# Kernel optimization log

Hardware: AMD Instinct MI355X
Metric: run time of the kernel (lower is better)

The kernel has to match this reference:

```python
import jax, jax.numpy as jnp
import numpy as np

B, T, D_MODEL = 2, 2048, 2048
N_HEAD, N_KV = 16, 4
HEAD_DIM = D_MODEL // N_HEAD  # 128
N_REP = N_HEAD // N_KV        # 4
ROPE_BASE = 10000.0


def setup_inputs() -> dict:
    key = jax.random.key(0)
    ks = jax.random.split(key, 5)
    s = 0.02
    return {
        "x": jax.random.normal(ks[0], (B, T, D_MODEL), dtype=jnp.float32),
        "Wq": jax.random.normal(ks[1], (D_MODEL, N_HEAD * HEAD_DIM), dtype=jnp.float32) * s,
        "Wk": jax.random.normal(ks[2], (D_MODEL, N_KV * HEAD_DIM), dtype=jnp.float32) * s,
        "Wv": jax.random.normal(ks[3], (D_MODEL, N_KV * HEAD_DIM), dtype=jnp.float32) * s,
        "Wo": jax.random.normal(ks[4], (D_MODEL, D_MODEL), dtype=jnp.float32) * s,
    }


def _rope_cos_sin(seq_len, dim, dtype):
    inv_freq = 1.0 / (ROPE_BASE ** (jnp.arange(0, dim, 2, dtype=jnp.float32) / dim))
    t = jnp.arange(seq_len, dtype=jnp.float32)
    freqs = t[:, None] * inv_freq[None, :]          # (T, dim/2)
    emb = jnp.concatenate([freqs, freqs], axis=-1)  # (T, dim)
    return jnp.cos(emb).astype(dtype), jnp.sin(emb).astype(dtype)


def _rotate_half(x):
    half = x.shape[-1] // 2
    return jnp.concatenate([-x[..., half:], x[..., :half]], axis=-1)


def reference(x, Wq, Wk, Wv, Wo):
    Bx, Tx, _ = x.shape
    # projections (weights stored (in, out); equals torch Linear with W^T)
    q = (x @ Wq).reshape(Bx, Tx, N_HEAD, HEAD_DIM).transpose(0, 2, 1, 3)  # (B,H,T,d)
    k = (x @ Wk).reshape(Bx, Tx, N_KV, HEAD_DIM).transpose(0, 2, 1, 3)    # (B,Hkv,T,d)
    v = (x @ Wv).reshape(Bx, Tx, N_KV, HEAD_DIM).transpose(0, 2, 1, 3)

    cos, sin = _rope_cos_sin(Tx, HEAD_DIM, x.dtype)  # (T, d)
    q = q * cos + _rotate_half(q) * sin
    k = k * cos + _rotate_half(k) * sin

    # grouped attention: q grouped by kv head, avoids materializing repeated K/V
    qg = q.reshape(Bx, N_KV, N_REP, Tx, HEAD_DIM)
    scale = 1.0 / np.sqrt(HEAD_DIM)
    att = jnp.einsum('bgrtd,bgsd->bgrts', qg, k) * scale  # (B,Hkv,rep,T,S)
    causal = jnp.tril(jnp.ones((Tx, Tx), dtype=bool))
    att = jnp.where(causal, att, -jnp.inf)
    att = jax.nn.softmax(att, axis=-1)
    y = jnp.einsum('bgrts,bgsd->bgrtd', att, v)           # (B,Hkv,rep,T,d)
    y = y.reshape(Bx, N_HEAD, Tx, HEAD_DIM).transpose(0, 2, 1, 3).reshape(Bx, Tx, D_MODEL)
    return y @ Wo
```

## Files before the change

kernel.cpp:

```cpp
#include <hip/hip_runtime.h>
#include <hip/hip_bf16.h>

typedef unsigned short u16;
typedef unsigned int u32;
typedef __attribute__((ext_vector_type(4))) float f32x4;
typedef __attribute__((ext_vector_type(8))) __bf16 bf16x8;

#define B_   2
#define T_   2048
#define DM   2048
#define NH   16
#define NKV  4
#define HD   128

__device__ __forceinline__ u16 f2bf(float f){
    u32 u = __builtin_bit_cast(u32, f);
    u += 0x7FFFu + ((u >> 16) & 1u);
    return (u16)(u >> 16);
}

__device__ __forceinline__ void gld_lds16(const void* g, void* l){
    __builtin_amdgcn_global_load_lds(
        (const __attribute__((address_space(1))) void*)g,
        (__attribute__((address_space(3))) void*)l, 16, 0, 0);
}

__global__ void cast_v4(const float* __restrict__ in, u16* __restrict__ out){
    int i = blockIdx.x * 256 + threadIdx.x;
    float4 v = ((const float4*)in)[i];
    ushort4 o;
    o.x = f2bf(v.x); o.y = f2bf(v.y); o.z = f2bf(v.z); o.w = f2bf(v.w);
    ((ushort4*)out)[i] = o;
}

__global__ void transAll(const float* __restrict__ Wq, const float* __restrict__ Wk,
                         const float* __restrict__ Wv, const float* __restrict__ Wo,
                         u16* __restrict__ Wqkv, u16* __restrict__ Wot){
    __shared__ float tile[32][33];
    int bx = blockIdx.x;
    const float* W; u16* Out; int N; int nb; int perm;
    if (bx < 64)      { W = Wq; Out = Wqkv;                  N = 2048; nb = bx;      perm = 1; }
    else if (bx < 80) { W = Wk; Out = Wqkv + 2048ull * 2048; N = 512;  nb = bx - 64; perm = 1; }
    else if (bx < 96) { W = Wv; Out = Wqkv + 2560ull * 2048; N = 512;  nb = bx - 80; perm = 0; }
    else              { W = Wo; Out = Wot;                   N = 2048; nb = bx - 96; perm = 0; }
    int n0 = nb * 32, k0 = blockIdx.y * 32;
    int tx = threadIdx.x, ty = threadIdx.y;
#pragma unroll
    for (int i = 0; i < 4; i++)
        tile[ty + i * 8][tx] = W[(size_t)(k0 + ty + i * 8) * N + n0 + tx];
    __syncthreads();
#pragma unroll
    for (int i = 0; i < 4; i++){
        int n = n0 + ty + i * 8;
        int np = perm ? ((n & ~127) | ((n & 63) << 1) | ((n >> 6) & 1)) : n;
        Out[(size_t)np * 2048 + k0 + tx] = f2bf(tile[tx][ty + i * 8]);
    }
}

__global__ void rope_tab(float2* __restrict__ tab){
    int idx = blockIdx.x * 256 + threadIdx.x;
    int i = idx & 63, t = idx >> 6;
    float ang = (float)t * exp2f((float)i * (-13.287712379549449f / 64.0f));
    float sv, cv;
    __sincosf(ang, &sv, &cv);
    tab[idx] = make_float2(cv, sv);
}

#define BARR() { __builtin_amdgcn_s_barrier(); __builtin_amdgcn_sched_barrier(0); }
#define LGKM0() { asm volatile("s_waitcnt lgkmcnt(0)" ::: "memory"); __builtin_amdgcn_sched_barrier(0); }
#define VM4() { asm volatile("s_waitcnt vmcnt(4)" ::: "memory"); __builtin_amdgcn_sched_barrier(0); }

#define READ_A(QA, BUF) { \
    const char* ab = (const char*)&As[BUF][wm][0]; \
    _Pragma("unroll") for (int i = 0; i < 4; i++){ \
        int rh = ((QA)*4 + i)*16 + lx; \
        _Pragma("unroll") for (int ks = 0; ks < 2; ks++) \
            a_[i][ks] = *(const bf16x8*)(ab + rh*128 + (((ks*4+tg)*16) ^ ((lx&7)<<4))); \
    } }
#define READ_B(QB, BUF) { \
    const char* bb = (const char*)&Bs[BUF][wn>>1][0]; \
    _Pragma("unroll") for (int n = 0; n < 2; n++){ \
        int rbh = (wn&1)*64 + ((QB)*2+n)*16 + lx; \
        _Pragma("unroll") for (int ks = 0; ks < 2; ks++) \
            b_[(QB)*2+n][ks] = *(const bf16x8*)(bb + rbh*128 + (((ks*4+tg)*16) ^ ((lx&7)<<4))); \
    } }
#define MFMA_Q(QA, QB) { \
    __builtin_amdgcn_s_setprio(1); \
    _Pragma("unroll") for (int i = 0; i < 4; i++) \
    _Pragma("unroll") for (int n = 0; n < 2; n++) \
    _Pragma("unroll") for (int ks = 0; ks < 2; ks++) \
        acc[(QA)*4+i][(QB)*2+n] = __builtin_amdgcn_mfma_f32_16x16x32_bf16( \
            a_[i][ks], b_[(QB)*2+n][ks], acc[(QA)*4+i][(QB)*2+n], 0, 0, 0); \
    __builtin_amdgcn_s_setprio(0); }

template<int MODE>
__global__ __launch_bounds__(512, 2) void gemm256(const u16* __restrict__ A, const u16* __restrict__ Bt,
                                                  void* __restrict__ O0, u16* __restrict__ Ktl,
                                                  u16* __restrict__ Vtl, const float2* __restrict__ tab,
                                                  int NBX){
    __shared__ __attribute__((aligned(16))) u16 As[2][2][8192];
    __shared__ __attribute__((aligned(16))) u16 Bs[2][2][8192];
    const int tid = threadIdx.x;
    const int lane = tid & 63, w = tid >> 6;
    const int wm = w >> 2, wn = w & 3;
    const int tg = lane >> 4, lx = lane & 15;
    int q8 = (int)gridDim.x >> 3;
    int swz = ((int)blockIdx.x & 7) * q8 + ((int)blockIdx.x >> 3);
    const int bx = swz % NBX, by = swz / NBX;
    const int m0 = by * 256, n0 = bx * 256;
    const int K = 2048;
    const int kcx = (lane & 7) ^ ((lane >> 3) & 7);

    f32x4 acc[8][4];
    const f32x4 Z = {0.f, 0.f, 0.f, 0.f};
#pragma unroll
    for (int i = 0; i < 8; i++)
#pragma unroll
        for (int j = 0; j < 4; j++) acc[i][j] = Z;
    bf16x8 a_[4][2], b_[4][2];

    auto stA = [&](int buf, int q, int kt){
        int mh = w >> 2;
        int s0 = (w & 3) * 2;
#pragma unroll
        for (int l = 0; l < 2; l++){
            int s = s0 + l;
            gld_lds16(A + (size_t)(m0 + mh*128 + q*64 + s*8 + (lane>>3)) * K + kt*64 + kcx*8,
                      &As[buf][mh][q*4096 + s*512 + lane*8]);
        }
    };
    auto stB = [&](int buf, int q, int kt){
        int bh = w >> 2;
        int hi = (w >> 1) & 1;
        int s0 = (w & 1) * 2;
#pragma unroll
        for (int l = 0; l < 2; l++){
            int s = s0 + l;
            gld_lds16(Bt + (size_t)(n0 + bh*128 + hi*64 + q*32 + s*8 + (lane>>3)) * K + kt*64 + kcx*8,
                      &Bs[buf][bh][hi*4096 + q*2048 + s*512 + lane*8]);
        }
    };

    stA(0, 0, 0); stB(0, 0, 0); stA(0, 1, 0); stB(0, 1, 0);
    stA(1, 0, 1); stB(1, 0, 1);
    VM4(); BARR();

#pragma unroll 1
    for (int it = 0; it < 16; it++){
        const int T1 = 2*it + 1;
        const int T2 = (2*it + 2 < 32) ? 2*it + 2 : 31;
        const int T3 = (2*it + 3 < 32) ? 2*it + 3 : 31;
        READ_A(0, 0); READ_B(0, 0); stA(1, 1, T1);
        BARR(); LGKM0(); MFMA_Q(0, 0); BARR();
        READ_B(1, 0); stB(1, 1, T1);
        BARR(); LGKM0(); MFMA_Q(0, 1); BARR();
        READ_A(1, 0); stA(0, 0, T2);
        BARR(); LGKM0(); MFMA_Q(1, 0); BARR();
        stB(0, 0, T2);
        BARR(); MFMA_Q(1, 1); VM4(); BARR();
        READ_A(0, 1); READ_B(0, 1); stA(0, 1, T2);
        BARR(); LGKM0(); MFMA_Q(0, 0); BARR();
        READ_B(1, 1); stB(0, 1, T2);
        BARR(); LGKM0(); MFMA_Q(0, 1); BARR();
        READ_A(1, 1); stA(1, 0, T3);
        BARR(); LGKM0(); MFMA_Q(1, 0); BARR();
        stB(1, 0, T3);
        BARR(); MFMA_Q(1, 1); VM4(); BARR();
    }

    if constexpr (MODE == 0){
        float* C = (float*)O0;
#pragma unroll
        for (int mi = 0; mi < 8; mi++)
#pragma unroll
            for (int ni = 0; ni < 4; ni++){
                int r0 = m0 + wm*128 + mi*16 + tg*4;
                int c  = n0 + wn*64 + ni*16 + lx;
#pragma unroll
                for (int j = 0; j < 4; j++)
                    C[(size_t)(r0 + j) * 2048 + c] = acc[mi][ni][j];
            }
    } else {
        u16* Qp = (u16*)O0;
        if (bx < 8){
#pragma unroll
            for (int mi = 0; mi < 8; mi++)
#pragma unroll
                for (int ni = 0; ni < 4; ni++){
                    int r0 = m0 + wm*128 + mi*16 + tg*4;
                    int c  = n0 + wn*64 + ni*16 + lx;
                    int ii = (c & 127) >> 1;
#pragma unroll
                    for (int j = 0; j < 4; j++){
                        float v = acc[mi][ni][j];
                        float p = __shfl_xor(v, 1);
                        int t = (r0 + j) & 2047;
                        float2 cs = tab[t * 64 + ii];
                        float o = (lx & 1) ? (v * cs.x + p * cs.y) : (v * cs.x - p * cs.y);
                        Qp[(size_t)(r0 + j) * 2048 + c] = f2bf(o);
                    }
                }
        } else if (bx < 10){
#pragma unroll
            for (int mi = 0; mi < 8; mi++)
#pragma unroll
                for (int ni = 0; ni < 4; ni++){
                    int r0 = m0 + wm*128 + mi*16 + tg*4;
                    int c  = n0 + wn*64 + ni*16 + lx;
                    int hk = (c >> 7) & 3;
                    int dd = c & 127;
                    int ii = dd >> 1;
#pragma unroll
                    for (int j = 0; j < 4; j++){
                        int r = r0 + j;
                        int bb2 = r >> 11, tt = r & 2047;
                        float v = acc[mi][ni][j];
                        float p = __shfl_xor(v, 1);
                        float2 cs = tab[tt * 64 + ii];
                        float o = (lx & 1) ? (v * cs.x + p * cs.y) : (v * cs.x - p * cs.y);
                        size_t tb = ((size_t)(bb2 * 4 + hk) * 32 + (tt >> 6)) * 8192;
                        u32 byte = (u32)((tt & 63) * 256) + (((u32)(2 * dd)) ^ ((u32)((tt & 7) << 4)));
                        Ktl[tb + byte / 2] = f2bf(o);
                    }
                }
        } else {
#pragma unroll
            for (int mi = 0; mi < 8; mi++){
                int r0 = m0 + wm*128 + mi*16 + tg*4;
                int bb2 = r0 >> 11, ss = r0 & 2047;
#pragma unroll
                for (int ni = 0; ni < 4; ni++){
                    int c  = n0 + wn*64 + ni*16 + lx;
                    int hk = (c >> 7) & 3;
                    int d  = c & 127;
                    size_t tb = ((size_t)(bb2 * 4 + hk) * 32 + (ss >> 6)) * 8192;
                    u32 byte = (u32)(d * 128) + (((u32)((ss & 63) * 2)) ^ ((u32)((d & 7) << 4)));
                    ushort4 o;
                    o.x = f2bf(acc[mi][ni][0]); o.y = f2bf(acc[mi][ni][1]);
                    o.z = f2bf(acc[mi][ni][2]); o.w = f2bf(acc[mi][ni][3]);
                    *(ushort4*)(Vtl + tb + byte / 2) = o;
                }
            }
        }
    }
}

__global__ __launch_bounds__(256) void attn4(const u16* __restrict__ Q, const u16* __restrict__ Kt,
                                             const u16* __restrict__ Vt, u16* __restrict__ Y){
    __shared__ __attribute__((aligned(16))) u16 Ks[2][64 * 128];
    __shared__ __attribute__((aligned(16))) u16 Vs[2][64 * 128];
    __shared__ __attribute__((aligned(16))) u16 Pl[4][16 * 64];
    const int lane = threadIdx.x & 63, w = threadIdx.x >> 6;
    const int jb = blockIdx.x, h = blockIdx.y, b = blockIdx.z;
    const int hkv = h >> 2;
    const size_t kvBase = ((size_t)(b * NKV + hkv) * 32) * 8192;
    const float scale = 0.08838834764831845f;
    const f32x4 Z = {0.f, 0.f, 0.f, 0.f};
    const int tg = lane >> 4, lx = lane & 15;

    auto STAGE = [&](int buf, int it){
        const u16* kg = Kt + kvBase + (size_t)it * 8192;
        const u16* vg = Vt + kvBase + (size_t)it * 8192;
#pragma unroll
        for (int i = 0; i < 4; i++){
            int is = w * 4 + i;
            gld_lds16(kg + is * 512 + lane * 8, &Ks[buf][is * 512]);
            gld_lds16(vg + is * 512 + lane * 8, &Vs[buf][is * 512]);
        }
    };

#pragma unroll 1
    for (int pass = 0; pass < 2; pass++){
        const int qt = pass == 0 ? jb : 31 - jb;
        const int q0 = qt * 64;
        const int qrow = q0 + w * 16 + lx;
        bf16x8 qfr[4];
#pragma unroll
        for (int kk = 0; kk < 4; kk++)
            qfr[kk] = *(const bf16x8*)(Q + (size_t)(b * T_ + qrow) * DM + h * HD + kk * 32 + tg * 8);
        f32x4 accO[8];
#pragma unroll
        for (int i = 0; i < 8; i++) accO[i] = Z;
        float mr[4] = {-INFINITY, -INFINITY, -INFINITY, -INFINITY};
        float lp[4] = {0.f, 0.f, 0.f, 0.f};
        const int nIter = qt + 1;

        STAGE(0, 0);
        __syncthreads();
        int cur = 0;

#pragma unroll 1
        for (int it = 0; it < nIter; it++){
            if (it + 1 < nIter) STAGE(cur ^ 1, it + 1);
            f32x4 sa[4];
#pragma unroll
            for (int c = 0; c < 4; c++) sa[c] = Z;
            __builtin_amdgcn_s_setprio(1);
#pragma unroll
            for (int c = 0; c < 4; c++){
                int s = c * 16 + lx;
                u32 swz = (u32)((s & 7) << 4);
                const char* kb = (const char*)&Ks[cur][0] + s * 256;
#pragma unroll
                for (int kk = 0; kk < 4; kk++){
                    bf16x8 kf = *(const bf16x8*)(kb + (((u32)(kk * 64 + tg * 16)) ^ swz));
                    sa[c] = __builtin_amdgcn_mfma_f32_16x16x32_bf16(qfr[kk], kf, sa[c], 0, 0, 0);
                }
            }
            __builtin_amdgcn_s_setprio(0);
            const bool diag = (it == nIter - 1);
            float rmax[4];
#pragma unroll
            for (int j = 0; j < 4; j++){
                float a0 = sa[0][j] * scale, a1 = sa[1][j] * scale;
                float a2 = sa[2][j] * scale, a3 = sa[3][j] * scale;
                if (diag){
                    int qloc = w * 16 + tg * 4 + j;
                    if (lx      > qloc) a0 = -INFINITY;
                    if (lx + 16 > qloc) a1 = -INFINITY;
                    if (lx + 32 > qloc) a2 = -INFINITY;
                    if (lx + 48 > qloc) a3 = -INFINITY;
                }
                sa[0][j] = a0; sa[1][j] = a1; sa[2][j] = a2; sa[3][j] = a3;
                float t = fmaxf(fmaxf(a0, a1), fmaxf(a2, a3));
                t = fmaxf(t, __shfl_xor(t, 1));
                t = fmaxf(t, __shfl_xor(t, 2));
                t = fmaxf(t, __shfl_xor(t, 4));
                t = fmaxf(t, __shfl_xor(t, 8));
                rmax[j] = t;
            }
            int lok = (rmax[0] <= mr[0] + 8.f) && (rmax[1] <= mr[1] + 8.f) &&
                      (rmax[2] <= mr[2] + 8.f) && (rmax[3] <= mr[3] + 8.f);
            const bool ok = __all(lok);
            float corr[4];
#pragma unroll
            for (int j = 0; j < 4; j++){
                float mn;
                if (!ok){
                    mn = fmaxf(mr[j], rmax[j]);
                    corr[j] = __expf(mr[j] - mn);
                    mr[j] = mn;
                } else {
                    mn = mr[j];
                }
                float p0 = __expf(sa[0][j] - mn), p1 = __expf(sa[1][j] - mn);
                float p2 = __expf(sa[2][j] - mn), p3 = __expf(sa[3][j] - mn);
                int rr = tg * 4 + j;
                u32 swz = (u32)((rr & 7) << 4);
                char* pb = (char*)&Pl[w][0] + rr * 128;
                u32 cb = (u32)(lx * 2);
                *(u16*)(pb + ((cb      ) ^ swz)) = f2bf(p0);
                *(u16*)(pb + ((cb + 32 ) ^ swz)) = f2bf(p1);
                *(u16*)(pb + ((cb + 64 ) ^ swz)) = f2bf(p2);
                *(u16*)(pb + ((cb + 96 ) ^ swz)) = f2bf(p3);
                lp[j] = (ok ? lp[j] : lp[j] * corr[j]) + (p0 + p1 + p2 + p3);
            }
            if (!ok){
#pragma unroll
                for (int dt = 0; dt < 8; dt++){
                    f32x4 t = accO[dt];
                    t[0] *= corr[0]; t[1] *= corr[1]; t[2] *= corr[2]; t[3] *= corr[3];
                    accO[dt] = t;
                }
            }
            bf16x8 pf[2];
            {
                char* pb = (char*)&Pl[w][0] + lx * 128;
                u32 swz = (u32)((lx & 7) << 4);
                pf[0] = *(const bf16x8*)(pb + (((u32)(tg * 16))      ^ swz));
                pf[1] = *(const bf16x8*)(pb + (((u32)(tg * 16 + 64)) ^ swz));
            }
            __builtin_amdgcn_s_setprio(1);
#pragma unroll
            for (int dt = 0; dt < 8; dt++){
                int d = dt * 16 + lx;
                u32 swz = (u32)((d & 7) << 4);
                const char* vb = (const char*)&Vs[cur][0] + d * 128;
                bf16x8 vf0 = *(const bf16x8*)(vb + (((u32)(tg * 16))      ^ swz));
                bf16x8 vf1 = *(const bf16x8*)(vb + (((u32)(tg * 16 + 64)) ^ swz));
                accO[dt] = __builtin_amdgcn_mfma_f32_16x16x32_bf16(pf[0], vf0, accO[dt], 0, 0, 0);
                accO[dt] = __builtin_amdgcn_mfma_f32_16x16x32_bf16(pf[1], vf1, accO[dt], 0, 0, 0);
            }
            __builtin_amdgcn_s_setprio(0);
            __syncthreads();
            cur ^= 1;
        }
        float inv[4];
#pragma unroll
        for (int j = 0; j < 4; j++){
            float s = lp[j];
            s += __shfl_xor(s, 1);
            s += __shfl_xor(s, 2);
            s += __shfl_xor(s, 4);
            s += __shfl_xor(s, 8);
            inv[j] = 1.0f / s;
        }
#pragma unroll
        for (int dt = 0; dt < 8; dt++)
#pragma unroll
            for (int j = 0; j < 4; j++){
                int qr = q0 + w * 16 + tg * 4 + j;
                int d = dt * 16 + lx;
                Y[(size_t)(b * T_ + qr) * DM + h * HD + d] = f2bf(accO[dt][j] * inv[j]);
            }
    }
}

extern "C" void kernel_launch(void* const* d_in, const int* in_sizes, int n_in,
                              void* d_out, int out_size, void* d_ws, size_t ws_size,
                              hipStream_t stream){
    const float* x  = (const float*)d_in[0];
    const float* Wq = (const float*)d_in[1];
    const float* Wk = (const float*)d_in[2];
    const float* Wv = (const float*)d_in[3];
    const float* Wo = (const float*)d_in[4];

    char* ws = (char*)d_ws;
    size_t off = 0;
    auto alloc = [&](size_t bytes){ void* p = ws + off; off += (bytes + 255) & ~255ull; return p; };
    u16*    xb   = (u16*)alloc(4096ull * 2048 * 2);
    u16*    Wqkv = (u16*)alloc(3072ull * 2048 * 2);
    u16*    Wot  = (u16*)alloc(2048ull * 2048 * 2);
    u16*    qbb  = (u16*)alloc(4096ull * 2048 * 2);
    u16*    ktl  = (u16*)alloc(2ull * 4 * 32 * 8192 * 2);
    u16*    vtl  = (u16*)alloc(2ull * 4 * 32 * 8192 * 2);
    u16*    ybb  = (u16*)alloc(4096ull * 2048 * 2);
    float2* tab  = (float2*)alloc(2048ull * 64 * 8);

    cast_v4<<<8192, 256, 0, stream>>>(x, xb);
    transAll<<<dim3(160, 64), dim3(32, 8), 0, stream>>>(Wq, Wk, Wv, Wo, Wqkv, Wot);
    rope_tab<<<512, 256, 0, stream>>>(tab);

    gemm256<1><<<192, 512, 0, stream>>>(xb, Wqkv, qbb, ktl, vtl, tab, 12);

    attn4<<<dim3(16, 16, 2), 256, 0, stream>>>(qbb, ktl, vtl, ybb);

    gemm256<0><<<128, 512, 0, stream>>>(ybb, Wot, d_out, nullptr, nullptr, nullptr, 8);
}
```

Measured before the change: 226.7 us.

## Fold softmax scale and log2e into Q, use exp2 and packed P stores

Pre-multiplies Q by scale*log2(e) in the projection epilogue so attention uses raw v_exp_f32 (exp2) with no per-score scaling. The row-max cross-lane shuffle reduction now runs only when the lazy rescale check fails. The P tile is written with packed bf16 conversions as one 8-byte store per row, and the V tile is stored with a permuted key order so P and V stay consistent. This cuts VALU and LDS work in the softmax inner loop. In exchange, V stores become scalar 2-byte writes, and the threshold now compares against a per-lane rather than a row max, in log2 units.

Result: faster. 216.2 us (-4.6%).

```diff
diff --git a/kernel.cpp b/kernel.cpp
--- a/kernel.cpp
+++ b/kernel.cpp
@@ -17,6 +17,10 @@
     u32 u = __builtin_bit_cast(u32, f);
     u += 0x7FFFu + ((u >> 16) & 1u);
     return (u16)(u >> 16);
+}
+
+__device__ __forceinline__ float ex2(float x){
+    float r; asm("v_exp_f32 %0, %1" : "=v"(r) : "v"(x)); return r;
 }
 
 __device__ __forceinline__ void gld_lds16(const void* g, void* l){
@@ -183,6 +187,7 @@
     } else {
         u16* Qp = (u16*)O0;
         if (bx < 8){
+            const float QS = 0.08838834764831845f * 1.4426950408889634f;
 #pragma unroll
             for (int mi = 0; mi < 8; mi++)
 #pragma unroll
@@ -196,7 +201,7 @@
                         float p = __shfl_xor(v, 1);
                         int t = (r0 + j) & 2047;
                         float2 cs = tab[t * 64 + ii];
-                        float o = (lx & 1) ? (v * cs.x + p * cs.y) : (v * cs.x - p * cs.y);
+                        float o = ((lx & 1) ? (v * cs.x + p * cs.y) : (v * cs.x - p * cs.y)) * QS;
                         Qp[(size_t)(r0 + j) * 2048 + c] = f2bf(o);
                     }
                 }
@@ -228,24 +233,28 @@
             for (int mi = 0; mi < 8; mi++){
                 int r0 = m0 + wm*128 + mi*16 + tg*4;
                 int bb2 = r0 >> 11, ss = r0 & 2047;
+                int sb = ss & 63;
 #pragma unroll
                 for (int ni = 0; ni < 4; ni++){
                     int c  = n0 + wn*64 + ni*16 + lx;
                     int hk = (c >> 7) & 3;
                     int d  = c & 127;
                     size_t tb = ((size_t)(bb2 * 4 + hk) * 32 + (ss >> 6)) * 8192;
-                    u32 byte = (u32)(d * 128) + (((u32)((ss & 63) * 2)) ^ ((u32)((d & 7) << 4)));
-                    ushort4 o;
-                    o.x = f2bf(acc[mi][ni][0]); o.y = f2bf(acc[mi][ni][1]);
-                    o.z = f2bf(acc[mi][ni][2]); o.w = f2bf(acc[mi][ni][3]);
-                    *(ushort4*)(Vtl + tb + byte / 2) = o;
+                    u32 swzd = (u32)((d & 7) << 4);
+#pragma unroll
+                    for (int j = 0; j < 4; j++){
+                        int s = sb + j;
+                        int sig = ((s & 15) << 2) | ((s >> 4) & 3);
+                        u32 byte = (u32)(d * 128) + (((u32)(2 * sig)) ^ swzd);
+                        Vtl[tb + byte / 2] = f2bf(acc[mi][ni][j]);
+                    }
                 }
             }
         }
     }
 }
 
-__global__ __launch_bounds__(256) void attn4(const u16* __restrict__ Q, const u16* __restrict__ Kt,
+__global__ __launch_bounds__(256) void attn5(const u16* __restrict__ Q, const u16* __restrict__ Kt,
                                              const u16* __restrict__ Vt, u16* __restrict__ Y){
     __shared__ __attribute__((aligned(16))) u16 Ks[2][64 * 128];
     __shared__ __attribute__((aligned(16))) u16 Vs[2][64 * 128];
@@ -254,7 +263,6 @@
     const int jb = blockIdx.x, h = blockIdx.y, b = blockIdx.z;
     const int hkv = h >> 2;
     const size_t kvBase = ((size_t)(b * NKV + hkv) * 32) * 8192;
-    const float scale = 0.08838834764831845f;
     const f32x4 Z = {0.f, 0.f, 0.f, 0.f};
     const int tg = lane >> 4, lx = lane & 15;
 
@@ -309,11 +317,10 @@
             }
             __builtin_amdgcn_s_setprio(0);
             const bool diag = (it == nIter - 1);
-            float rmax[4];
+            float tl[4];
 #pragma unroll
             for (int j = 0; j < 4; j++){
-                float a0 = sa[0][j] * scale, a1 = sa[1][j] * scale;
-                float a2 = sa[2][j] * scale, a3 = sa[3][j] * scale;
+                float a0 = sa[0][j], a1 = sa[1][j], a2 = sa[2][j], a3 = sa[3][j];
                 if (diag){
                     int qloc = w * 16 + tg * 4 + j;
                     if (lx      > qloc) a0 = -INFINITY;
@@ -322,46 +329,44 @@
                     if (lx + 48 > qloc) a3 = -INFINITY;
                 }
                 sa[0][j] = a0; sa[1][j] = a1; sa[2][j] = a2; sa[3][j] = a3;
-                float t = fmaxf(fmaxf(a0, a1), fmaxf(a2, a3));
-                t = fmaxf(t, __shfl_xor(t, 1));
-                t = fmaxf(t, __shfl_xor(t, 2));
-                t = fmaxf(t, __shfl_xor(t, 4));
-                t = fmaxf(t, __shfl_xor(t, 8));
-                rmax[j] = t;
-            }
-            int lok = (rmax[0] <= mr[0] + 8.f) && (rmax[1] <= mr[1] + 8.f) &&
-                      (rmax[2] <= mr[2] + 8.f) && (rmax[3] <= mr[3] + 8.f);
-            const bool ok = __all(lok);
-            float corr[4];
-#pragma unroll
-            for (int j = 0; j < 4; j++){
-                float mn;
-                if (!ok){
-                    mn = fmaxf(mr[j], rmax[j]);
-                    corr[j] = __expf(mr[j] - mn);
+                tl[j] = fmaxf(fmaxf(a0, a1), fmaxf(a2, a3));
+            }
+            int lok = (tl[0] <= mr[0] + 8.f) && (tl[1] <= mr[1] + 8.f) &&
+                      (tl[2] <= mr[2] + 8.f) && (tl[3] <= mr[3] + 8.f);
+            if (!__all(lok)){
+                float corr[4];
+#pragma unroll
+                for (int j = 0; j < 4; j++){
+                    float t = tl[j];
+                    t = fmaxf(t, __shfl_xor(t, 1));
+                    t = fmaxf(t, __shfl_xor(t, 2));
+                    t = fmaxf(t, __shfl_xor(t, 4));
+                    t = fmaxf(t, __shfl_xor(t, 8));
+                    float mn = fmaxf(mr[j], t);
+                    corr[j] = ex2(mr[j] - mn);
                     mr[j] = mn;
-                } else {
-                    mn = mr[j];
-                }
-                float p0 = __expf(sa[0][j] - mn), p1 = __expf(sa[1][j] - mn);
-                float p2 = __expf(sa[2][j] - mn), p3 = __expf(sa[3][j] - mn);
-                int rr = tg * 4 + j;
-                u32 swz = (u32)((rr & 7) << 4);
-                char* pb = (char*)&Pl[w][0] + rr * 128;
-                u32 cb = (u32)(lx * 2);
-                *(u16*)(pb + ((cb      ) ^ swz)) = f2bf(p0);
-                *(u16*)(pb + ((cb + 32 ) ^ swz)) = f2bf(p1);
-                *(u16*)(pb + ((cb + 64 ) ^ swz)) = f2bf(p2);
-                *(u16*)(pb + ((cb + 96 ) ^ swz)) = f2bf(p3);
-                lp[j] = (ok ? lp[j] : lp[j] * corr[j]) + (p0 + p1 + p2 + p3);
-            }
-            if (!ok){
+                    lp[j] *= corr[j];
+                }
 #pragma unroll
                 for (int dt = 0; dt < 8; dt++){
                     f32x4 t = accO[dt];
                     t[0] *= corr[0]; t[1] *= corr[1]; t[2] *= corr[2]; t[3] *= corr[3];
                     accO[dt] = t;
                 }
+            }
+#pragma unroll
+            for (int j = 0; j < 4; j++){
+                float mn = mr[j];
+                float p0 = ex2(sa[0][j] - mn), p1 = ex2(sa[1][j] - mn);
+                float p2 = ex2(sa[2][j] - mn), p3 = ex2(sa[3][j] - mn);
+                lp[j] += p0 + p1 + p2 + p3;
+                int rr = tg * 4 + j;
+                u32 woff = (u32)(rr * 128) + (((u32)(lx * 8)) ^ ((u32)((rr & 7) << 4)));
+                u32 r01, r23;
+                asm("v_cvt_pk_bf16_f32 %0, %1, %2" : "=v"(r01) : "v"(p0), "v"(p1));
+                asm("v_cvt_pk_bf16_f32 %0, %1, %2" : "=v"(r23) : "v"(p2), "v"(p3));
+                uint2 pk2 = make_uint2(r01, r23);
+                *(uint2*)((char*)&Pl[w][0] + woff) = pk2;
             }
             bf16x8 pf[2];
             {
@@ -433,7 +438,7 @@
 
     gemm256<1><<<192, 512, 0, stream>>>(xb, Wqkv, qbb, ktl, vtl, tab, 12);
 
-    attn4<<<dim3(16, 16, 2), 256, 0, stream>>>(qbb, ktl, vtl, ybb);
+    attn5<<<dim3(16, 16, 2), 256, 0, stream>>>(qbb, ktl, vtl, ybb);
 
     gemm256<0><<<128, 512, 0, stream>>>(ybb, Wot, d_out, nullptr, nullptr, nullptr, 8);
 }
```
